# Optimization experiments

Hardware: AMD Instinct MI355X
Metric: run time of the kernel (lower is better)

Reference implementation:

```python
import jax, jax.numpy as jnp
import numpy as np

K = 3          # kernel size (hardcoded in module)
PAD = 1        # kernel_size // 2
K2 = K * K


def conv3x3(x, w, b):
    """Standard 3x3 stride-1 same-padding conv, NCHW / OIHW."""
    y = jax.lax.conv_general_dilated(
        x, w, window_strides=(1, 1), padding=[(PAD, PAD), (PAD, PAD)],
        dimension_numbers=('NCHW', 'OIHW', 'NCHW'))
    return y + b[None, :, None, None]


def setup_inputs() -> dict:
    key = jax.random.key(0)
    ks = jax.random.split(key, 8)
    B, C, O, H, W = 8, 64, 64, 128, 128
    x = jax.random.normal(ks[0], (B, C, H, W), dtype=jnp.float32)
    # offset conv: 2*K2 output channels; small init so offsets stay modest
    w_off = jax.random.normal(ks[1], (2 * K2, C, K, K), dtype=jnp.float32) * 0.05
    b_off = jnp.zeros((2 * K2,), dtype=jnp.float32)
    # modulator conv: K2 output channels
    w_mod = jax.random.normal(ks[2], (K2, C, K, K), dtype=jnp.float32) * 0.05
    b_mod = jnp.zeros((K2,), dtype=jnp.float32)
    # main deformable conv weight/bias
    w = jax.random.normal(ks[3], (O, C, K, K), dtype=jnp.float32) * (1.0 / np.sqrt(C * K2))
    b = jax.random.normal(ks[4], (O,), dtype=jnp.float32) * 0.01
    return {"x": x, "w_off": w_off, "b_off": b_off,
            "w_mod": w_mod, "b_mod": b_mod, "w": w, "b": b}


def reference(x, w_off, b_off, w_mod, b_mod, w, b):
    B, C, H, W = x.shape
    O = w.shape[0]

    # offset / modulator heads (torchvision layout: channel 2k = dy, 2k+1 = dx)
    offset = conv3x3(x, w_off, b_off)                       # [B, 2*K2, H, W]
    mask = 2.0 * jax.nn.sigmoid(conv3x3(x, w_mod, b_mod))   # [B, K2, H, W]
    off = offset.reshape(B, K2, 2, H, W)
    dy, dx = off[:, :, 0], off[:, :, 1]                     # [B, K2, H, W]

    # base sampling grid: p = (h - pad + ki, w - pad + kj) + learned offset
    ki = (jnp.arange(K2) // K).astype(x.dtype)
    kj = (jnp.arange(K2) % K).astype(x.dtype)
    hh = jnp.arange(H, dtype=x.dtype)
    ww = jnp.arange(W, dtype=x.dtype)
    py = dy + hh[None, None, :, None] - PAD + ki[None, :, None, None]
    px = dx + ww[None, None, None, :] - PAD + kj[None, :, None, None]

    def sample_one(x_b, py_b, px_b):
        # x_b: [C, H, W]; py_b, px_b: [K2, H, W]. Bilinear, zero outside.
        y0 = jnp.floor(py_b)
        x0 = jnp.floor(px_b)
        wy = py_b - y0                                      # [K2, H, W]
        wx = px_b - x0
        y0i = y0.astype(jnp.int32)
        x0i = x0.astype(jnp.int32)

        def gather(yi, xi):
            valid = (yi >= 0) & (yi < H) & (xi >= 0) & (xi < W)
            v = x_b[:, jnp.clip(yi, 0, H - 1), jnp.clip(xi, 0, W - 1)]  # [C,K2,H,W]
            return v * valid[None].astype(x_b.dtype)

        v00 = gather(y0i, x0i)
        v01 = gather(y0i, x0i + 1)
        v10 = gather(y0i + 1, x0i)
        v11 = gather(y0i + 1, x0i + 1)
        return (v00 * (1 - wy) * (1 - wx) + v01 * (1 - wy) * wx
                + v10 * wy * (1 - wx) + v11 * wy * wx)       # [C, K2, H, W]

    sampled = jax.vmap(sample_one)(x, py, px)               # [B, C, K2, H, W]

    # modulated contraction over (c, k): GEMM-like core
    wk = w.reshape(O, C, K2)
    out = jnp.einsum('bckhw,bkhw,ock->bohw', sampled, mask, wk)
    return out + b[None, :, None, None]
```

## Files before the change

### kernel.cpp

```cpp
#include <hip/hip_runtime.h>
#include <math.h>

#define H_ 128
#define W_ 128
#define C_ 64
#define O_ 64
#define B_ 8
#define K2_ 9
#define HWSZ (H_*W_)

typedef float f2u __attribute__((ext_vector_type(2), aligned(4)));

__global__ __launch_bounds__(256) void prep_weights_k(
    const float* __restrict__ w, const float* __restrict__ w_off,
    const float* __restrict__ w_mod, float* __restrict__ wt,
    float* __restrict__ wom) {
    int id = blockIdx.x * 256 + threadIdx.x;
    if (id < K2_ * C_ * O_) {
        int o = id & (O_ - 1);
        int c = (id >> 6) & (C_ - 1);
        int k = id / (C_ * O_);
        wt[id] = w[(o * C_ + c) * K2_ + k];
    }
    int id2 = id - K2_ * C_ * O_;
    if (id2 >= 0 && id2 < C_ * 252) {
        int k = id2 % 9;
        int tt = (id2 / 9) % 28;
        int c = id2 / 252;
        float v = 0.0f;
        if (tt < 18)      v = w_off[(tt * C_ + c) * K2_ + k];
        else if (tt < 27) v = w_mod[((tt - 18) * C_ + c) * K2_ + k];
        wom[id2] = v;
    }
}

__global__ __launch_bounds__(512, 4) void conv_offmask_k(
    const float* __restrict__ x,
    const float* __restrict__ wom, const float* __restrict__ b_off,
    const float* __restrict__ b_mod,
    float* __restrict__ pyA, float* __restrict__ pxA, float* __restrict__ mA) {
    __shared__ float AO[28 * 256];

    int b     = blockIdx.x & 7;
    int strip = blockIdx.x >> 3;
    int tid   = threadIdx.x;
    int t     = tid & 127;
    int q     = tid >> 7;
    int qu    = __builtin_amdgcn_readfirstlane(q);
    int h0    = strip * 2;

    int offs[12]; float valid[12];
#pragma unroll
    for (int r = 0; r < 4; r++) {
#pragma unroll
        for (int cx = 0; cx < 3; cx++) {
            int yy = h0 - 1 + r, xx = t - 1 + cx;
            bool vv = (yy >= 0 && yy < H_ && xx >= 0 && xx < W_);
            int yc = min(max(yy, 0), H_ - 1);
            int xc = min(max(xx, 0), W_ - 1);
            offs[r * 3 + cx] = yc * W_ + xc;
            valid[r * 3 + cx] = vv ? 1.0f : 0.0f;
        }
    }

    float acc0[7], acc1[7];
#pragma unroll
    for (int o = 0; o < 7; o++) { acc0[o] = 0.0f; acc1[o] = 0.0f; }

    const float* xb = x + b * C_ * HWSZ;

    float v[12];
#pragma unroll
    for (int i = 0; i < 12; i++) v[i] = xb[offs[i]] * valid[i];

    for (int c = 0; c < C_; c++) {
        const float* xn = xb + min(c + 1, C_ - 1) * HWSZ;
        float vn[12];
#pragma unroll
        for (int i = 0; i < 12; i++) vn[i] = xn[offs[i]] * valid[i];

        const float* wq = wom + c * 252 + qu * 63;
#pragma unroll
        for (int o = 0; o < 7; o++) {
#pragma unroll
            for (int kk = 0; kk < 9; kk++) {
                float wv = wq[o * 9 + kk];
                int ki = kk / 3, kj = kk % 3;
                acc0[o] += v[ki * 3 + kj] * wv;
                acc1[o] += v[(ki + 1) * 3 + kj] * wv;
            }
        }
#pragma unroll
        for (int i = 0; i < 12; i++) v[i] = vn[i];
    }

#pragma unroll
    for (int o = 0; o < 7; o++) {
        AO[(qu * 7 + o) * 256 + t]       = acc0[o];
        AO[(qu * 7 + o) * 256 + 128 + t] = acc1[o];
    }
    __syncthreads();

    if (tid < 256) {
        int px = tid;
        int hh = h0 + (px >> 7);
        int ww = px & 127;
        int p  = hh * W_ + ww;
#pragma unroll
        for (int k = 0; k < 9; k++) {
            float dy = AO[(2 * k) * 256 + px]     + b_off[2 * k];
            float dx = AO[(2 * k + 1) * 256 + px] + b_off[2 * k + 1];
            float mm = AO[(18 + k) * 256 + px]    + b_mod[k];
            float mask = 2.0f / (1.0f + __expf(-mm));
            float py = dy + (float)hh - 1.0f + (float)(k / 3);
            float px_ = dx + (float)ww - 1.0f + (float)(k % 3);
            int idx = (b * 9 + k) * HWSZ + p;
            pyA[idx] = py;
            pxA[idx] = px_;
            mA[idx] = mask;
        }
    }
}

__global__ __launch_bounds__(512) void sample_gemm_k(
    const float* __restrict__ x,
    const float* __restrict__ pyA, const float* __restrict__ pxA,
    const float* __restrict__ mA, const float* __restrict__ wt,
    const float* __restrict__ bias, float* __restrict__ out) {
    __shared__ float red[O_ * 256];

    int b     = blockIdx.x & 7;
    int strip = blockIdx.x >> 3;
    int tid   = threadIdx.x;
    int t     = tid & 255;
    int half  = tid >> 8;
    int c0    = __builtin_amdgcn_readfirstlane(half << 5);
    int p     = strip * 256 + t;

    float acc[O_];
#pragma unroll
    for (int o = 0; o < O_; o++) acc[o] = 0.0f;

    const float* xb = x + (b * C_ + c0) * HWSZ;

    for (int k = 0; k < 9; k++) {
        int idx = (b * 9 + k) * HWSZ + p;
        float py = pyA[idx];
        float px = pxA[idx];
        float m  = mA[idx];

        float y0f = floorf(py), x0f = floorf(px);
        float wy = py - y0f, wx = px - x0f;
        int y0 = (int)y0f, x0 = (int)x0f;
        int y1 = y0 + 1;
        float vy0 = (y0 >= 0 && y0 < H_) ? 1.0f : 0.0f;
        float vy1 = (y1 >= 0 && y1 < H_) ? 1.0f : 0.0f;
        float vx0 = (x0 >= 0 && x0 < W_) ? 1.0f : 0.0f;
        float vx1 = (x0 >= -1 && x0 < W_ - 1) ? 1.0f : 0.0f;
        int y0c = min(max(y0, 0), H_ - 1), y1c = min(max(y1, 0), H_ - 1);

        float w00 = (1.0f - wy) * (1.0f - wx) * vy0 * vx0 * m;
        float w01 = (1.0f - wy) * wx * vy0 * vx1 * m;
        float w10 = wy * (1.0f - wx) * vy1 * vx0 * m;
        float w11 = wy * wx * vy1 * vx1 * m;

        int lc   = min(max(x0, 0), W_ - 2);
        bool xlo = (x0 < 0);
        bool xhi = (x0 > W_ - 2);
        float a00 = xhi ? 0.0f : (xlo ? w01 : w00);
        float a01 = xlo ? 0.0f : (xhi ? w00 : w01);
        float a10 = xhi ? 0.0f : (xlo ? w11 : w10);
        float a11 = xlo ? 0.0f : (xhi ? w10 : w11);

        int r0 = y0c * W_ + lc;
        int r1 = y1c * W_ + lc;

        const float* wp = wt + k * (C_ * O_) + c0 * O_;
        for (int c = 0; c < 32; c++) {
            const float* xc = xb + c * HWSZ;
            f2u f0 = *(const f2u*)(xc + r0);
            f2u f1 = *(const f2u*)(xc + r1);
            float s = a00 * f0.x + a01 * f0.y + a10 * f1.x + a11 * f1.y;
            const float* wpc = wp + c * O_;
#pragma unroll
            for (int o = 0; o < O_; o++) acc[o] += s * wpc[o];
        }
    }

    if (half) {
#pragma unroll
        for (int o = 0; o < O_; o++) red[o * 256 + t] = acc[o];
    }
    __syncthreads();
    if (!half) {
        int obase = b * O_ * HWSZ + p;
#pragma unroll
        for (int o = 0; o < O_; o++)
            out[obase + o * HWSZ] = acc[o] + red[o * 256 + t] + bias[o];
    }
}

extern "C" void kernel_launch(void* const* d_in, const int* in_sizes, int n_in,
                              void* d_out, int out_size, void* d_ws, size_t ws_size,
                              hipStream_t stream) {
    const float* x     = (const float*)d_in[0];
    const float* w_off = (const float*)d_in[1];
    const float* b_off = (const float*)d_in[2];
    const float* w_mod = (const float*)d_in[3];
    const float* b_mod = (const float*)d_in[4];
    const float* w     = (const float*)d_in[5];
    const float* bias  = (const float*)d_in[6];
    float* out = (float*)d_out;

    const int nCoord = B_ * K2_ * HWSZ;
    float* pyA = (float*)d_ws;
    float* pxA = pyA + nCoord;
    float* mA  = pxA + nCoord;
    float* wt  = mA + nCoord;
    float* wom = wt + K2_ * C_ * O_;

    const int nPrep = K2_ * C_ * O_ + C_ * 252;
    hipLaunchKernelGGL(prep_weights_k, dim3((nPrep + 255) / 256), dim3(256),
                       0, stream, w, w_off, w_mod, wt, wom);
    hipLaunchKernelGGL(conv_offmask_k, dim3(512), dim3(512), 0, stream,
                       x, wom, b_off, b_mod, pyA, pxA, mA);
    hipLaunchKernelGGL(sample_gemm_k, dim3(512), dim3(512), 0, stream,
                       x, pyA, pxA, mA, wt, bias, out);
}
```

Before: 303.6 us.

## Restructure offset conv: 2x2 outputs per thread, split channels across halves

The offset/mask conv kernel now computes a 2x2 output patch per thread. It loads 4-wide row vectors, so each weight load feeds four FMAs instead of two and the neighbouring pixel values are reused. The 64 input channels are split between two thread halves, and the partial sums are reduced through shared memory. This cuts global loads and weight reads per FMA, at the cost of an extra shared-memory reduction pass and sync, plus more registers.

```diff
diff --git a/kernel.cpp b/kernel.cpp
--- a/kernel.cpp
+++ b/kernel.cpp
@@ -10,6 +10,7 @@
 #define HWSZ (H_*W_)
 
 typedef float f2u __attribute__((ext_vector_type(2), aligned(4)));
+typedef float f4u __attribute__((ext_vector_type(4), aligned(4)));
 
 __global__ __launch_bounds__(256) void prep_weights_k(
     const float* __restrict__ w, const float* __restrict__ w_off,
@@ -44,60 +45,89 @@
     int b     = blockIdx.x & 7;
     int strip = blockIdx.x >> 3;
     int tid   = threadIdx.x;
-    int t     = tid & 127;
-    int q     = tid >> 7;
-    int qu    = __builtin_amdgcn_readfirstlane(q);
+    int u     = tid & 63;
+    int oq    = (tid >> 6) & 3;
+    int chh   = tid >> 8;
+    int qu    = __builtin_amdgcn_readfirstlane(oq);
+    int hu    = __builtin_amdgcn_readfirstlane(chh);
     int h0    = strip * 2;
 
-    int offs[12]; float valid[12];
+    int   yc[4]; float vval[4];
 #pragma unroll
     for (int r = 0; r < 4; r++) {
-#pragma unroll
-        for (int cx = 0; cx < 3; cx++) {
-            int yy = h0 - 1 + r, xx = t - 1 + cx;
-            bool vv = (yy >= 0 && yy < H_ && xx >= 0 && xx < W_);
-            int yc = min(max(yy, 0), H_ - 1);
-            int xc = min(max(xx, 0), W_ - 1);
-            offs[r * 3 + cx] = yc * W_ + xc;
-            valid[r * 3 + cx] = vv ? 1.0f : 0.0f;
-        }
-    }
-
-    float acc0[7], acc1[7];
-#pragma unroll
-    for (int o = 0; o < 7; o++) { acc0[o] = 0.0f; acc1[o] = 0.0f; }
-
-    const float* xb = x + b * C_ * HWSZ;
-
-    float v[12];
-#pragma unroll
-    for (int i = 0; i < 12; i++) v[i] = xb[offs[i]] * valid[i];
-
-    for (int c = 0; c < C_; c++) {
-        const float* xn = xb + min(c + 1, C_ - 1) * HWSZ;
-        float vn[12];
-#pragma unroll
-        for (int i = 0; i < 12; i++) vn[i] = xn[offs[i]] * valid[i];
-
-        const float* wq = wom + c * 252 + qu * 63;
+        int yy = h0 - 1 + r;
+        vval[r] = (yy >= 0 && yy < H_) ? 1.0f : 0.0f;
+        yc[r] = min(max(yy, 0), H_ - 1);
+    }
+    int  lc  = min(max(2 * u - 1, 0), W_ - 4);
+    bool u0  = (u == 0);
+    bool u63 = (u == 63);
+
+    const float* xb = x + (b * C_ + hu * 32) * HWSZ;
+
+    float acc[7][4];
+#pragma unroll
+    for (int o = 0; o < 7; o++)
+#pragma unroll
+        for (int j = 0; j < 4; j++) acc[o][j] = 0.0f;
+
+    f4u L[4];
+#pragma unroll
+    for (int r = 0; r < 4; r++)
+        L[r] = *(const f4u*)(xb + yc[r] * W_ + lc);
+
+    for (int c = 0; c < 32; c++) {
+        const float* xn = xb + min(c + 1, 31) * HWSZ;
+        f4u Ln[4];
+#pragma unroll
+        for (int r = 0; r < 4; r++)
+            Ln[r] = *(const f4u*)(xn + yc[r] * W_ + lc);
+
+        float v[4][4];
+#pragma unroll
+        for (int r = 0; r < 4; r++) {
+            float l0 = L[r].x, l1 = L[r].y, l2 = L[r].z, l3 = L[r].w;
+            v[r][0] = (u0 ? 0.0f : (u63 ? l1 : l0)) * vval[r];
+            v[r][1] = (u0 ? l0   : (u63 ? l2 : l1)) * vval[r];
+            v[r][2] = (u0 ? l1   : (u63 ? l3 : l2)) * vval[r];
+            v[r][3] = (u0 ? l2   : (u63 ? 0.0f : l3)) * vval[r];
+        }
+
+        const float* wq = wom + (hu * 32 + c) * 252 + qu * 63;
 #pragma unroll
         for (int o = 0; o < 7; o++) {
 #pragma unroll
             for (int kk = 0; kk < 9; kk++) {
                 float wv = wq[o * 9 + kk];
                 int ki = kk / 3, kj = kk % 3;
-                acc0[o] += v[ki * 3 + kj] * wv;
-                acc1[o] += v[(ki + 1) * 3 + kj] * wv;
+                acc[o][0] += v[ki][kj]     * wv;
+                acc[o][1] += v[ki][kj + 1] * wv;
+                acc[o][2] += v[ki + 1][kj]     * wv;
+                acc[o][3] += v[ki + 1][kj + 1] * wv;
             }
         }
 #pragma unroll
-        for (int i = 0; i < 12; i++) v[i] = vn[i];
-    }
-
-#pragma unroll
-    for (int o = 0; o < 7; o++) {
-        AO[(qu * 7 + o) * 256 + t]       = acc0[o];
-        AO[(qu * 7 + o) * 256 + 128 + t] = acc1[o];
+        for (int r = 0; r < 4; r++) L[r] = Ln[r];
+    }
+
+    float2* AO2 = (float2*)AO;
+    if (chh == 1) {
+#pragma unroll
+        for (int o = 0; o < 7; o++) {
+            AO2[(qu * 7 + o) * 128 + u]      = make_float2(acc[o][0], acc[o][1]);
+            AO2[(qu * 7 + o) * 128 + 64 + u] = make_float2(acc[o][2], acc[o][3]);
+        }
+    }
+    __syncthreads();
+    if (chh == 0) {
+#pragma unroll
+        for (int o = 0; o < 7; o++) {
+            int i0 = (qu * 7 + o) * 128 + u;
+            float2 t0 = AO2[i0], t1 = AO2[i0 + 64];
+            t0.x += acc[o][0]; t0.y += acc[o][1];
+            t1.x += acc[o][2]; t1.y += acc[o][3];
+            AO2[i0] = t0; AO2[i0 + 64] = t1;
+        }
     }
     __syncthreads();
 
```

New measurement: 297.3 us. 1.02x faster.

## Restructure offset/mask conv to one row per block with vector loads

Applied to the files above, without the earlier changes.

The offset/modulator conv kernel now has each block process a single output row instead of two, doubling the grid to 1024 blocks and raising the occupancy hint. Each thread loads three 4-wide vectors per channel (rows above, at, and below) and selects the three taps with edge handling, replacing twelve scalar loads and the software prefetch. This cuts per-thread registers and raises parallelism. In exchange, the vertical halo rows are reloaded by adjacent blocks and each loaded value is reused across fewer output rows.

```diff
diff --git a/kernel.cpp b/kernel.cpp
--- a/kernel.cpp
+++ b/kernel.cpp
@@ -10,6 +10,7 @@
 #define HWSZ (H_*W_)
 
 typedef float f2u __attribute__((ext_vector_type(2), aligned(4)));
+typedef float f4u __attribute__((ext_vector_type(4), aligned(4)));
 
 __global__ __launch_bounds__(256) void prep_weights_k(
     const float* __restrict__ w, const float* __restrict__ w_off,
@@ -34,89 +35,81 @@
     }
 }
 
-__global__ __launch_bounds__(512, 4) void conv_offmask_k(
+__global__ __launch_bounds__(512, 8) void conv_offmask_k(
     const float* __restrict__ x,
     const float* __restrict__ wom, const float* __restrict__ b_off,
     const float* __restrict__ b_mod,
     float* __restrict__ pyA, float* __restrict__ pxA, float* __restrict__ mA) {
-    __shared__ float AO[28 * 256];
-
-    int b     = blockIdx.x & 7;
-    int strip = blockIdx.x >> 3;
-    int tid   = threadIdx.x;
-    int t     = tid & 127;
-    int q     = tid >> 7;
-    int qu    = __builtin_amdgcn_readfirstlane(q);
-    int h0    = strip * 2;
-
-    int offs[12]; float valid[12];
-#pragma unroll
-    for (int r = 0; r < 4; r++) {
-#pragma unroll
-        for (int cx = 0; cx < 3; cx++) {
-            int yy = h0 - 1 + r, xx = t - 1 + cx;
-            bool vv = (yy >= 0 && yy < H_ && xx >= 0 && xx < W_);
-            int yc = min(max(yy, 0), H_ - 1);
-            int xc = min(max(xx, 0), W_ - 1);
-            offs[r * 3 + cx] = yc * W_ + xc;
-            valid[r * 3 + cx] = vv ? 1.0f : 0.0f;
-        }
-    }
-
-    float acc0[7], acc1[7];
-#pragma unroll
-    for (int o = 0; o < 7; o++) { acc0[o] = 0.0f; acc1[o] = 0.0f; }
+    __shared__ float AO[28 * 128];
+
+    int b    = blockIdx.x & 7;
+    int hrow = blockIdx.x >> 3;
+    int tid  = threadIdx.x;
+    int t    = tid & 127;
+    int oq   = tid >> 7;
+    int qu   = __builtin_amdgcn_readfirstlane(oq);
+
+    int   yc0 = max(hrow - 1, 0);
+    int   yc2 = min(hrow + 1, H_ - 1);
+    float va0 = (hrow > 0) ? 1.0f : 0.0f;
+    float va2 = (hrow < H_ - 1) ? 1.0f : 0.0f;
+
+    int  lc   = min(max(t - 1, 0), W_ - 4);
+    bool t0   = (t == 0);
+    bool t126 = (t == 126);
+    bool t127 = (t == 127);
 
     const float* xb = x + b * C_ * HWSZ;
 
-    float v[12];
-#pragma unroll
-    for (int i = 0; i < 12; i++) v[i] = xb[offs[i]] * valid[i];
+    float acc[7];
+#pragma unroll
+    for (int o = 0; o < 7; o++) acc[o] = 0.0f;
 
     for (int c = 0; c < C_; c++) {
-        const float* xn = xb + min(c + 1, C_ - 1) * HWSZ;
-        float vn[12];
-#pragma unroll
-        for (int i = 0; i < 12; i++) vn[i] = xn[offs[i]] * valid[i];
+        const float* xc = xb + c * HWSZ;
+        f4u L0 = *(const f4u*)(xc + yc0  * W_ + lc);
+        f4u L1 = *(const f4u*)(xc + hrow * W_ + lc);
+        f4u L2 = *(const f4u*)(xc + yc2  * W_ + lc);
+
+        float v[9];
+#define TAPS(R, LR, VM)                                                        \
+        {                                                                      \
+            float l0 = LR.x, l1 = LR.y, l2 = LR.z, l3 = LR.w;                  \
+            v[(R)*3+0] = (t0 ? 0.0f : (t127 ? l2 : (t126 ? l1 : l0))) * (VM);  \
+            v[(R)*3+1] = (t0 ? l0   : (t127 ? l3 : (t126 ? l2 : l1))) * (VM);  \
+            v[(R)*3+2] = (t0 ? l1   : (t127 ? 0.0f : (t126 ? l3 : l2))) * (VM);\
+        }
+        TAPS(0, L0, va0)
+        TAPS(1, L1, 1.0f)
+        TAPS(2, L2, va2)
+#undef TAPS
 
         const float* wq = wom + c * 252 + qu * 63;
 #pragma unroll
         for (int o = 0; o < 7; o++) {
 #pragma unroll
-            for (int kk = 0; kk < 9; kk++) {
-                float wv = wq[o * 9 + kk];
-                int ki = kk / 3, kj = kk % 3;
-                acc0[o] += v[ki * 3 + kj] * wv;
-                acc1[o] += v[(ki + 1) * 3 + kj] * wv;
-            }
-        }
-#pragma unroll
-        for (int i = 0; i < 12; i++) v[i] = vn[i];
-    }
-
-#pragma unroll
-    for (int o = 0; o < 7; o++) {
-        AO[(qu * 7 + o) * 256 + t]       = acc0[o];
-        AO[(qu * 7 + o) * 256 + 128 + t] = acc1[o];
-    }
+            for (int kk = 0; kk < 9; kk++)
+                acc[o] += v[kk] * wq[o * 9 + kk];
+        }
+    }
+
+#pragma unroll
+    for (int o = 0; o < 7; o++) AO[(qu * 7 + o) * 128 + t] = acc[o];
     __syncthreads();
 
-    if (tid < 256) {
-        int px = tid;
-        int hh = h0 + (px >> 7);
-        int ww = px & 127;
-        int p  = hh * W_ + ww;
+    if (tid < 128) {
+        int p = hrow * W_ + t;
 #pragma unroll
         for (int k = 0; k < 9; k++) {
-            float dy = AO[(2 * k) * 256 + px]     + b_off[2 * k];
-            float dx = AO[(2 * k + 1) * 256 + px] + b_off[2 * k + 1];
-            float mm = AO[(18 + k) * 256 + px]    + b_mod[k];
+            float dy = AO[(2 * k) * 128 + t]     + b_off[2 * k];
+            float dx = AO[(2 * k + 1) * 128 + t] + b_off[2 * k + 1];
+            float mm = AO[(18 + k) * 128 + t]    + b_mod[k];
             float mask = 2.0f / (1.0f + __expf(-mm));
-            float py = dy + (float)hh - 1.0f + (float)(k / 3);
-            float px_ = dx + (float)ww - 1.0f + (float)(k % 3);
+            float py = dy + (float)hrow - 1.0f + (float)(k / 3);
+            float px = dx + (float)t - 1.0f + (float)(k % 3);
             int idx = (b * 9 + k) * HWSZ + p;
             pyA[idx] = py;
-            pxA[idx] = px_;
+            pxA[idx] = px;
             mA[idx] = mask;
         }
     }
@@ -222,7 +215,7 @@
     const int nPrep = K2_ * C_ * O_ + C_ * 252;
     hipLaunchKernelGGL(prep_weights_k, dim3((nPrep + 255) / 256), dim3(256),
                        0, stream, w, w_off, w_mod, wt, wom);
-    hipLaunchKernelGGL(conv_offmask_k, dim3(512), dim3(512), 0, stream,
+    hipLaunchKernelGGL(conv_offmask_k, dim3(1024), dim3(512), 0, stream,
                        x, wom, b_off, b_mod, pyA, pxA, mA);
     hipLaunchKernelGGL(sample_gemm_k, dim3(512), dim3(512), 0, stream,
                        x, pyA, pxA, mA, wt, bias, out);
```

New measurement: 338.7 us. 1.12x slower.

## Vectorize offset/mask conv loads and double-buffer weights in registers

Applied to the files above, without the earlier changes.

Pads the packed offset/modulator weight table to 64 floats per quarter so each wave can load its weights as 16 float4 vectors into registers. Input rows are fetched as one float4 per row with boundary lanes remapped by selects, instead of 12 scalar masked gathers. Weights and tiles are double-buffered across channel pairs to overlap loads with FMAs. Occupancy hint drops from 4 to 2 blocks per CU, which raises register pressure headroom but may cut latency hiding.

```diff
diff --git a/kernel.cpp b/kernel.cpp
--- a/kernel.cpp
+++ b/kernel.cpp
@@ -10,6 +10,7 @@
 #define HWSZ (H_*W_)
 
 typedef float f2u __attribute__((ext_vector_type(2), aligned(4)));
+typedef float f4u __attribute__((ext_vector_type(4), aligned(4)));
 
 __global__ __launch_bounds__(256) void prep_weights_k(
     const float* __restrict__ w, const float* __restrict__ w_off,
@@ -23,18 +24,23 @@
         wt[id] = w[(o * C_ + c) * K2_ + k];
     }
     int id2 = id - K2_ * C_ * O_;
-    if (id2 >= 0 && id2 < C_ * 252) {
-        int k = id2 % 9;
-        int tt = (id2 / 9) % 28;
-        int c = id2 / 252;
+    if (id2 >= 0 && id2 < C_ * 256) {
+        int c = id2 >> 8;
+        int rr = id2 & 255;
+        int q = rr >> 6;
+        int r = rr & 63;
         float v = 0.0f;
-        if (tt < 18)      v = w_off[(tt * C_ + c) * K2_ + k];
-        else if (tt < 27) v = w_mod[((tt - 18) * C_ + c) * K2_ + k];
+        if (r < 63) {
+            int tt = q * 7 + r / 9;
+            int k  = r % 9;
+            if (tt < 18)      v = w_off[(tt * C_ + c) * K2_ + k];
+            else if (tt < 27) v = w_mod[((tt - 18) * C_ + c) * K2_ + k];
+        }
         wom[id2] = v;
     }
 }
 
-__global__ __launch_bounds__(512, 4) void conv_offmask_k(
+__global__ __launch_bounds__(512, 2) void conv_offmask_k(
     const float* __restrict__ x,
     const float* __restrict__ wom, const float* __restrict__ b_off,
     const float* __restrict__ b_mod,
@@ -45,59 +51,99 @@
     int strip = blockIdx.x >> 3;
     int tid   = threadIdx.x;
     int t     = tid & 127;
-    int q     = tid >> 7;
-    int qu    = __builtin_amdgcn_readfirstlane(q);
+    int oq    = tid >> 7;
+    int qu    = __builtin_amdgcn_readfirstlane(oq);
+    int qoff  = qu * 64;
     int h0    = strip * 2;
 
-    int offs[12]; float valid[12];
-#pragma unroll
-    for (int r = 0; r < 4; r++) {
-#pragma unroll
-        for (int cx = 0; cx < 3; cx++) {
-            int yy = h0 - 1 + r, xx = t - 1 + cx;
-            bool vv = (yy >= 0 && yy < H_ && xx >= 0 && xx < W_);
-            int yc = min(max(yy, 0), H_ - 1);
-            int xc = min(max(xx, 0), W_ - 1);
-            offs[r * 3 + cx] = yc * W_ + xc;
-            valid[r * 3 + cx] = vv ? 1.0f : 0.0f;
-        }
-    }
-
-    float acc0[7], acc1[7];
-#pragma unroll
-    for (int o = 0; o < 7; o++) { acc0[o] = 0.0f; acc1[o] = 0.0f; }
+    int lz = __builtin_amdgcn_mbcnt_lo(0u, 0u);
+    const float* womv = wom + lz;
+
+    int   yc0 = max(h0 - 1, 0);
+    int   yc3 = min(h0 + 2, H_ - 1);
+    float vv[4];
+    vv[0] = (h0 > 0) ? 1.0f : 0.0f;
+    vv[1] = 1.0f;
+    vv[2] = 1.0f;
+    vv[3] = (h0 + 2 < H_) ? 1.0f : 0.0f;
+
+    int  lc   = min(max(t - 1, 0), W_ - 4);
+    bool t0   = (t == 0);
+    bool t126 = (t == 126);
+    bool t127 = (t == 127);
 
     const float* xb = x + b * C_ * HWSZ;
 
-    float v[12];
-#pragma unroll
-    for (int i = 0; i < 12; i++) v[i] = xb[offs[i]] * valid[i];
-
-    for (int c = 0; c < C_; c++) {
-        const float* xn = xb + min(c + 1, C_ - 1) * HWSZ;
-        float vn[12];
-#pragma unroll
-        for (int i = 0; i < 12; i++) vn[i] = xn[offs[i]] * valid[i];
-
-        const float* wq = wom + c * 252 + qu * 63;
-#pragma unroll
-        for (int o = 0; o < 7; o++) {
-#pragma unroll
-            for (int kk = 0; kk < 9; kk++) {
-                float wv = wq[o * 9 + kk];
-                int ki = kk / 3, kj = kk % 3;
-                acc0[o] += v[ki * 3 + kj] * wv;
-                acc1[o] += v[(ki + 1) * 3 + kj] * wv;
-            }
-        }
-#pragma unroll
-        for (int i = 0; i < 12; i++) v[i] = vn[i];
-    }
+    float acc[7][2];
+#pragma unroll
+    for (int o = 0; o < 7; o++) { acc[o][0] = 0.0f; acc[o][1] = 0.0f; }
+
+#define WGET(WW, WI)                                                           \
+    (((WI) & 3) == 0 ? WW[(WI) >> 2].x : ((WI) & 3) == 1 ? WW[(WI) >> 2].y :   \
+     ((WI) & 3) == 2 ? WW[(WI) >> 2].z : WW[(WI) >> 2].w)
+
+#define WLOAD(DST, CC)                                                         \
+    {                                                                          \
+        const float* wp_ = womv + (CC) * 256 + qoff;                           \
+        _Pragma("unroll")                                                      \
+        for (int j = 0; j < 16; j++) DST[j] = *(const f4u*)(wp_ + 4 * j);      \
+    }
+
+#define TLOAD(DST, CC)                                                         \
+    {                                                                          \
+        const float* xc_ = xb + (CC) * HWSZ;                                   \
+        DST[0] = *(const f4u*)(xc_ + yc0 * W_ + lc);                           \
+        DST[1] = *(const f4u*)(xc_ + h0 * W_ + lc);                            \
+        DST[2] = *(const f4u*)(xc_ + (h0 + 1) * W_ + lc);                      \
+        DST[3] = *(const f4u*)(xc_ + yc3 * W_ + lc);                           \
+    }
+
+#define FMABODY(WW, TT)                                                        \
+    {                                                                          \
+        float v[4][3];                                                         \
+        _Pragma("unroll")                                                      \
+        for (int r = 0; r < 4; r++) {                                          \
+            float l0 = TT[r].x, l1 = TT[r].y, l2 = TT[r].z, l3 = TT[r].w;      \
+            float vm = vv[r];                                                  \
+            v[r][0] = (t0 ? 0.0f : (t127 ? l2 : (t126 ? l1 : l0))) * vm;       \
+            v[r][1] = (t0 ? l0   : (t127 ? l3 : (t126 ? l2 : l1))) * vm;       \
+            v[r][2] = (t0 ? l1   : (t127 ? 0.0f : (t126 ? l3 : l2))) * vm;     \
+        }                                                                      \
+        _Pragma("unroll")                                                      \
+        for (int o = 0; o < 7; o++) {                                          \
+            _Pragma("unroll")                                                  \
+            for (int kk = 0; kk < 9; kk++) {                                   \
+                const int wi = o * 9 + kk;                                     \
+                const int ki = kk / 3, kj = kk % 3;                            \
+                float wv = WGET(WW, wi);                                       \
+                acc[o][0] += v[ki][kj] * wv;                                   \
+                acc[o][1] += v[ki + 1][kj] * wv;                               \
+            }                                                                  \
+        }                                                                      \
+    }
+
+    f4u Wa[16], Wb[16], Ta[4], Tb[4];
+    WLOAD(Wa, 0)
+    TLOAD(Ta, 0)
+    for (int cc = 0; cc < 32; cc++) {
+        int ce = 2 * cc;
+        WLOAD(Wb, ce + 1)
+        TLOAD(Tb, ce + 1)
+        FMABODY(Wa, Ta)
+        int cn = (cc < 31) ? ce + 2 : 63;
+        WLOAD(Wa, cn)
+        TLOAD(Ta, cn)
+        FMABODY(Wb, Tb)
+    }
+#undef FMABODY
+#undef TLOAD
+#undef WLOAD
+#undef WGET
 
 #pragma unroll
     for (int o = 0; o < 7; o++) {
-        AO[(qu * 7 + o) * 256 + t]       = acc0[o];
-        AO[(qu * 7 + o) * 256 + 128 + t] = acc1[o];
+        AO[(qu * 7 + o) * 256 + t]       = acc[o][0];
+        AO[(qu * 7 + o) * 256 + 128 + t] = acc[o][1];
     }
     __syncthreads();
 
@@ -219,7 +265,7 @@
     float* wt  = mA + nCoord;
     float* wom = wt + K2_ * C_ * O_;
 
-    const int nPrep = K2_ * C_ * O_ + C_ * 252;
+    const int nPrep = K2_ * C_ * O_ + C_ * 256;
     hipLaunchKernelGGL(prep_weights_k, dim3((nPrep + 255) / 256), dim3(256),
                        0, stream, w, w_off, w_mod, wt, wom);
     hipLaunchKernelGGL(conv_offmask_k, dim3(512), dim3(512), 0, stream,
```

Result: slower. 505.5 us (+66.5%).
